# Optimization experiments

Hardware: AMD Instinct MI355X
Metric: run time of the kernel (lower is better)

## Reference

```python
import jax, jax.numpy as jnp
import numpy as np

N = 100000      # nodes_num
E = 1600000     # edges (avg degree 16)
D_IN = 256
D_OUT = 128
EPS = 1e-3      # keras BatchNormalization default epsilon
LEAKY = 0.2     # tf.nn.leaky_relu default alpha


def setup_inputs() -> dict:
    key = jax.random.key(0)
    ks = jax.random.split(key, 6)
    x = jax.random.normal(ks[0], (N, D_IN), jnp.float32)
    w = jax.random.normal(ks[1], (D_IN, D_OUT), jnp.float32) / np.float32(np.sqrt(D_IN))
    w1 = jax.random.normal(ks[2], (D_IN, D_IN), jnp.float32) / np.float32(np.sqrt(D_IN))
    w2 = jax.random.normal(ks[3], (D_IN, D_IN), jnp.float32) / np.float32(np.sqrt(D_IN))
    rows = jnp.sort(jax.random.randint(ks[4], (E,), 0, N, jnp.int32))
    cols = jax.random.randint(ks[5], (E,), 0, N, jnp.int32)
    edge_vals = jnp.ones((E,), jnp.float32)
    return {"x": x, "w": w, "w1": w1, "w2": w2,
            "edge_vals": edge_vals, "rows": rows, "cols": cols}


def reference(x, w, w1, w2, edge_vals, rows, cols):
    # Batch norm (training mode: per-feature stats over node axis, gamma=1, beta=0)
    mean = jnp.mean(x, axis=0)
    var = jnp.var(x, axis=0)
    xn = (x - mean) * jax.lax.rsqrt(var + EPS)          # [N, D_IN]

    mapped = xn @ w                                      # [N, D_OUT]
    s1 = jnp.tanh(jnp.sum((xn @ w1) * xn, axis=1))       # [N] row score
    s2 = jnp.tanh(jnp.sum((xn @ w2) * xn, axis=1))       # [N] col score

    # sparse add of adj*s1[row] and adj*s2[col], then leaky_relu on edge values
    ev = edge_vals * (s1[rows] + s2[cols])               # [E]
    ev = jnp.where(ev > 0, ev, LEAKY * ev)

    # tf.sparse.softmax: softmax over the nonzero entries of each row
    m = jax.ops.segment_max(ev, rows, num_segments=N)    # [N]
    m = jnp.where(jnp.isfinite(m), m, 0.0)               # empty rows -> 0
    ex = jnp.exp(ev - m[rows])
    denom = jax.ops.segment_sum(ex, rows, num_segments=N)
    alpha = ex / denom[rows]                             # [E] edge softmax

    # SpMM: out[i] = sum_{e: rows[e]==i} alpha[e] * mapped[cols[e]]
    out = jax.ops.segment_sum(alpha[:, None] * mapped[cols], rows, num_segments=N)
    return out  # activation is identity (activation=None)
```

## Files before the change

### kernel.cpp

```cpp
#include <hip/hip_runtime.h>

#define D_IN 256
#define D_OUT 128
#define EPS_BN 1e-3f
#define LEAKY 0.2f

typedef unsigned short u16;
typedef unsigned int u32;
typedef u16 u16x4 __attribute__((ext_vector_type(4)));
typedef u16 u16x8 __attribute__((ext_vector_type(8)));
typedef __bf16 bf16x8 __attribute__((ext_vector_type(8)));
typedef float f32x4 __attribute__((ext_vector_type(4)));

__device__ __forceinline__ float bf2f(u16 u) {
    u32 v = ((u32)u) << 16;
    return __uint_as_float(v);
}
__device__ __forceinline__ u16 f2bf(float f) {
    u32 u = __float_as_uint(f);
    u32 r = (u + 0x7FFFu + ((u >> 16) & 1u)) >> 16;
    return (u16)r;
}

__device__ __forceinline__ void bar_lgkm() {
    asm volatile("s_waitcnt lgkmcnt(0)" ::: "memory");
    __builtin_amdgcn_s_barrier();
    asm volatile("" ::: "memory");
}

__global__ void colstats_k(const float* __restrict__ x, int n,
                           float* __restrict__ sums, float* __restrict__ sqs) {
    int c = threadIdx.x;
    float s = 0.f, q = 0.f;
    for (int r = blockIdx.x; r < n; r += gridDim.x) {
        float v = x[(size_t)r * D_IN + c];
        s += v;
        q += v * v;
    }
    atomicAdd(&sums[c], s);
    atomicAdd(&sqs[c], q);
}

__global__ void finalize_k(const float* __restrict__ sums, const float* __restrict__ sqs,
                           int n, float* __restrict__ mean, float* __restrict__ inv) {
    int c = threadIdx.x;
    float m = sums[c] / (float)n;
    float v = sqs[c] / (float)n - m * m;
    mean[c] = m;
    inv[c] = rsqrtf(v + EPS_BN);
}

__global__ void prep_w_k(const float* __restrict__ w1, const float* __restrict__ w2,
                         const float* __restrict__ w, u16* __restrict__ Bth,
                         u16* __restrict__ Btl, u16* __restrict__ Wth,
                         u16* __restrict__ Wtl) {
    int idx = blockIdx.x * 256 + threadIdx.x;
    int k = idx & 255;
    int nn = idx >> 8;
    if (nn < 512) {
        float v = (nn < 256) ? w1[(size_t)k * 256 + nn]
                             : w2[(size_t)k * 256 + (nn - 256)];
        u16 h = f2bf(v);
        u16 l = f2bf(v - bf2f(h));
        Bth[(size_t)nn * 256 + k] = h;
        Btl[(size_t)nn * 256 + k] = l;
    } else {
        int nm = nn - 512;
        float v = w[(size_t)k * D_OUT + nm];
        u16 h = f2bf(v);
        u16 l = f2bf(v - bf2f(h));
        Wth[(size_t)nm * 256 + k] = h;
        Wtl[(size_t)nm * 256 + k] = l;
    }
}

__device__ __forceinline__ int kmap(int v, int g, int j) {
    return (v == 0) ? (8 * g + j) : (16 * (j >> 2) + 4 * g + (j & 3));
}

__global__ void probe_k(int* __restrict__ flagp) {
    __shared__ float Ar[16][32];
    __shared__ float Br[32][16];
    __shared__ float Dr[16][16];
    int l = threadIdx.x;
    for (int i = l; i < 512; i += 64) {
        int r = i >> 5, k = i & 31;
        Ar[r][k] = (float)(((r * 5 + k * 3) % 11) - 5);
    }
    for (int i = l; i < 512; i += 64) {
        int k = i >> 4, c = i & 15;
        Br[k][c] = (float)(((k * 3 + c * 7) % 13) - 6);
    }
    __syncthreads();
    for (int i = l; i < 256; i += 64) {
        int r = i >> 4, c = i & 15;
        float s = 0.f;
        for (int k = 0; k < 32; ++k) s += Ar[r][k] * Br[k][c];
        Dr[r][c] = s;
    }
    __syncthreads();
    int g = l >> 4, c15 = l & 15;
    int found = -1;
    for (int combo = 0; combo < 4; ++combo) {
        int va = combo >> 1, vb = combo & 1;
        u16x8 af, bfv;
#pragma unroll
        for (int j = 0; j < 8; ++j) {
            af[j] = f2bf(Ar[c15][kmap(va, g, j)]);
            bfv[j] = f2bf(Br[kmap(vb, g, j)][c15]);
        }
        f32x4 d = {0.f, 0.f, 0.f, 0.f};
        d = __builtin_amdgcn_mfma_f32_16x16x32_bf16(
            __builtin_bit_cast(bf16x8, af), __builtin_bit_cast(bf16x8, bfv), d,
            0, 0, 0);
        bool ok = true;
#pragma unroll
        for (int r = 0; r < 4; ++r) ok = ok && (d[r] == Dr[g * 4 + r][c15]);
        if (found < 0 && __all(ok)) found = combo;
    }
    if (l == 0) flagp[0] = (found < 0) ? 0 : found;
}

template <int NT>
__device__ __forceinline__ void stage_A(const float* __restrict__ x,
                                        const float* __restrict__ mean,
                                        const float* __restrict__ inv, int m0,
                                        int n, u16* Ah, u16* Al) {
    const int tid = threadIdx.x;
#pragma unroll
    for (int i = 0; i < 4096 / NT; ++i) {
        int chunk = tid + i * NT;
        int r = chunk >> 6;
        int c4 = (chunk & 63) << 2;
        int gr = m0 + r;
        bool ok = gr < n;
        float4 v = make_float4(0.f, 0.f, 0.f, 0.f);
        if (ok) v = *(const float4*)(x + (size_t)gr * D_IN + c4);
        float4 mn = *(const float4*)(mean + c4);
        float4 iv = *(const float4*)(inv + c4);
        float a0 = ok ? (v.x - mn.x) * iv.x : 0.f;
        float a1 = ok ? (v.y - mn.y) * iv.y : 0.f;
        float a2 = ok ? (v.z - mn.z) * iv.z : 0.f;
        float a3 = ok ? (v.w - mn.w) * iv.w : 0.f;
        u16 h0 = f2bf(a0), h1 = f2bf(a1), h2 = f2bf(a2), h3 = f2bf(a3);
        u16 l0 = f2bf(a0 - bf2f(h0)), l1 = f2bf(a1 - bf2f(h1));
        u16 l2 = f2bf(a2 - bf2f(h2)), l3 = f2bf(a3 - bf2f(h3));
        int off = (r << 9) + (((c4 << 1) ^ ((r & 7) << 4)));
        u16x4 hv = {h0, h1, h2, h3};
        u16x4 lv = {l0, l1, l2, l3};
        *(u16x4*)((char*)Ah + off) = hv;
        *(u16x4*)((char*)Al + off) = lv;
    }
}

template <int V>
__device__ __forceinline__ bf16x8 ld_frag(const u16* plane, int rowByteBase,
                                          int swz, int kbyte, int g) {
    const char* p = (const char*)plane + rowByteBase;
    if constexpr (V == 0) {
        u16x8 v = *(const u16x8*)(p + ((kbyte + (g << 4)) ^ swz));
        return __builtin_bit_cast(bf16x8, v);
    } else {
        u16x4 a = *(const u16x4*)(p + ((kbyte + (g << 3)) ^ swz));
        u16x4 b = *(const u16x4*)(p + ((kbyte + 32 + (g << 3)) ^ swz));
        u16x8 v;
        v[0] = a[0]; v[1] = a[1]; v[2] = a[2]; v[3] = a[3];
        v[4] = b[0]; v[5] = b[1]; v[6] = b[2]; v[7] = b[3];
        return __builtin_bit_cast(bf16x8, v);
    }
}

__device__ __forceinline__ void ldb2(const u16* __restrict__ Gh,
                                     const u16* __restrict__ Gl, int n0, int k0,
                                     int tid, u16x8 (&hv)[2], u16x8 (&lv)[2]) {
#pragma unroll
    for (int i = 0; i < 2; ++i) {
        int chunk = tid + (i << 8);
        int nl = chunk >> 2;
        int k8 = (chunk & 3) << 3;
        size_t goff = (size_t)(n0 + nl) * 256 + k0 + k8;
        hv[i] = *(const u16x8*)(Gh + goff);
        lv[i] = *(const u16x8*)(Gl + goff);
    }
}
__device__ __forceinline__ void stb2(u16* Bh, u16* Bl, int tid,
                                     const u16x8 (&hv)[2], const u16x8 (&lv)[2]) {
#pragma unroll
    for (int i = 0; i < 2; ++i) {
        int chunk = tid + (i << 8);
        int nl = chunk >> 2;
        int kb = (chunk & 3) << 4;
        int off = (nl << 6) + (kb ^ (((nl >> 1) & 3) << 4));
        *(u16x8*)((char*)Bh + off) = hv[i];
        *(u16x8*)((char*)Bl + off) = lv[i];
    }
}
template <int V>
__device__ __forceinline__ bf16x8 ld_bfrag(const u16* Bp, int nl, int g) {
    const char* p = (const char*)Bp + (nl << 6);
    int swz = ((nl >> 1) & 3) << 4;
    if constexpr (V == 0) {
        u16x8 v = *(const u16x8*)(p + ((g << 4) ^ swz));
        return __builtin_bit_cast(bf16x8, v);
    } else {
        u16x4 a = *(const u16x4*)(p + ((g << 3) ^ swz));
        u16x4 b = *(const u16x4*)(p + ((32 + (g << 3)) ^ swz));
        u16x8 v;
        v[0] = a[0]; v[1] = a[1]; v[2] = a[2]; v[3] = a[3];
        v[4] = b[0]; v[5] = b[1]; v[6] = b[2]; v[7] = b[3];
        return __builtin_bit_cast(bf16x8, v);
    }
}

template <int VA, int VB>
__device__ __forceinline__ void comp32(const u16* Ah, const u16* Al,
                                       const u16* Bh, const u16* Bl, int kbA,
                                       int wm, int wj, int c15, int g,
                                       f32x4 (&acc)[2][4]) {
    bf16x8 ah[2], alf[2];
#pragma unroll
    for (int mf = 0; mf < 2; ++mf) {
        int row = wm * 32 + mf * 16 + c15;
        int swz = (row & 7) << 4;
        ah[mf] = ld_frag<VA>(Ah, row << 9, swz, kbA, g);
        alf[mf] = ld_frag<VA>(Al, row << 9, swz, kbA, g);
    }
    bf16x8 bh[4], bl[4];
#pragma unroll
    for (int nf = 0; nf < 4; ++nf) {
        int nl = wj * 64 + nf * 16 + c15;
        bh[nf] = ld_bfrag<VB>(Bh, nl, g);
        bl[nf] = ld_bfrag<VB>(Bl, nl, g);
    }
#pragma unroll
    for (int mf = 0; mf < 2; ++mf)
#pragma unroll
        for (int nf = 0; nf < 4; ++nf) {
            acc[mf][nf] = __builtin_amdgcn_mfma_f32_16x16x32_bf16(
                ah[mf], bh[nf], acc[mf][nf], 0, 0, 0);
            acc[mf][nf] = __builtin_amdgcn_mfma_f32_16x16x32_bf16(
                ah[mf], bl[nf], acc[mf][nf], 0, 0, 0);
            acc[mf][nf] = __builtin_amdgcn_mfma_f32_16x16x32_bf16(
                alf[mf], bh[nf], acc[mf][nf], 0, 0, 0);
        }
}

__device__ __forceinline__ void nxt_src2(int u, int totSub,
                                         const u16* __restrict__ Bth,
                                         const u16* __restrict__ Btl,
                                         const u16* __restrict__ Wth,
                                         const u16* __restrict__ Wtl,
                                         const u16*& Gh, const u16*& Gl,
                                         int& n0, int& k0) {
    if (u >= totSub) u = totSub - 1;
    if (u < 32) {
        Gh = Bth; Gl = Btl;
        n0 = (u >> 3) << 7;
        k0 = (u & 7) << 5;
    } else {
        Gh = Wth; Gl = Wtl;
        n0 = 0;
        k0 = (u & 7) << 5;
    }
}

template <int VA, int VB>
__device__ __forceinline__ void quadmap_body(
    const float* __restrict__ x, const u16* __restrict__ Bth,
    const u16* __restrict__ Btl, const u16* __restrict__ Wth,
    const u16* __restrict__ Wtl, const float* __restrict__ mean,
    const float* __restrict__ inv, float* __restrict__ s1,
    float* __restrict__ s2, u16* __restrict__ mapped, int n, int mapCT,
    u16* Ah, u16* Al, u16* Bh, u16* Bl) {
    const int tid = threadIdx.x;
    const int lane = tid & 63, wave = tid >> 6;
    const int g = lane >> 4, c15 = lane & 15;
    const int wm = wave >> 1, wj = wave & 1;
    const int m0 = blockIdx.x * 64;

    stage_A<256>(x, mean, inv, m0, n, Ah, Al);
    __syncthreads();

    const int totSub = 32 + ((mapCT == 128) ? 8 : 0);
    u16x8 rh[2], rl[2];
    {
        const u16 *Gh, *Gl; int n0, k0;
        nxt_src2(0, totSub, Bth, Btl, Wth, Wtl, Gh, Gl, n0, k0);
        ldb2(Gh, Gl, n0, k0, tid, rh, rl);
    }

    float sp[2][4] = {{0.f, 0.f, 0.f, 0.f}, {0.f, 0.f, 0.f, 0.f}};
    float* red = (float*)Bh;

    for (int p = 0; p < 4; ++p) {
        f32x4 acc[2][4];
#pragma unroll
        for (int mf = 0; mf < 2; ++mf)
#pragma unroll
            for (int nf = 0; nf < 4; ++nf) acc[mf][nf] = (f32x4){0.f, 0.f, 0.f, 0.f};

#pragma unroll
        for (int u8 = 0; u8 < 8; ++u8) {
            bar_lgkm();
            stb2(Bh, Bl, tid, rh, rl);
            const u16 *Gh, *Gl; int n0, k0;
            nxt_src2(p * 8 + u8 + 1, totSub, Bth, Btl, Wth, Wtl, Gh, Gl, n0, k0);
            ldb2(Gh, Gl, n0, k0, tid, rh, rl);
            bar_lgkm();
            comp32<VA, VB>(Ah, Al, Bh, Bl, u8 * 64, wm, wj, c15, g, acc);
        }

        {
            int jtg = p * 2 + wj;
            int fcol0 = (jtg & 3) << 6;
#pragma unroll
            for (int nf = 0; nf < 4; ++nf) {
                int col = fcol0 + nf * 16 + c15;
                float mn = mean[col], ivv = inv[col];
#pragma unroll
                for (int mf = 0; mf < 2; ++mf) {
#pragma unroll
                    for (int r = 0; r < 4; ++r) {
                        int grow = m0 + wm * 32 + mf * 16 + g * 4 + r;
                        float xv = 0.f;
                        if (grow < n) xv = (x[(size_t)grow * D_IN + col] - mn) * ivv;
                        sp[mf][r] = fmaf(acc[mf][nf][r], xv, sp[mf][r]);
                    }
                }
            }
        }
        if (p & 1) {
            float part[2][4];
#pragma unroll
            for (int mf = 0; mf < 2; ++mf)
#pragma unroll
                for (int r = 0; r < 4; ++r) {
                    float v = sp[mf][r];
                    v += __shfl_xor(v, 1);
                    v += __shfl_xor(v, 2);
                    v += __shfl_xor(v, 4);
                    v += __shfl_xor(v, 8);
                    part[mf][r] = v;
                    sp[mf][r] = 0.f;
                }
            bar_lgkm();
            if (c15 == 0) {
#pragma unroll
                for (int mf = 0; mf < 2; ++mf)
#pragma unroll
                    for (int r = 0; r < 4; ++r) {
                        int sidx = (((((wm << 2) | g) << 1) | mf) << 3) | (r << 1) | wj;
                        red[sidx] = part[mf][r];
                    }
            }
            bar_lgkm();
            if (wj == 0 && c15 == 0) {
                float* dst = (p < 2) ? s1 : s2;
#pragma unroll
                for (int mf = 0; mf < 2; ++mf)
#pragma unroll
                    for (int r = 0; r < 4; ++r) {
                        int sidx = (((((wm << 2) | g) << 1) | mf) << 3) | (r << 1);
                        float tot = red[sidx] + red[sidx | 1];
                        int grow = m0 + wm * 32 + mf * 16 + g * 4 + r;
                        if (grow < n) dst[grow] = tanhf(tot);
                    }
            }
        }
    }

    if (mapCT == 128) {
        f32x4 acc[2][4];
#pragma unroll
        for (int mf = 0; mf < 2; ++mf)
#pragma unroll
            for (int nf = 0; nf < 4; ++nf) acc[mf][nf] = (f32x4){0.f, 0.f, 0.f, 0.f};

#pragma unroll
        for (int u8 = 0; u8 < 8; ++u8) {
            bar_lgkm();
            stb2(Bh, Bl, tid, rh, rl);
            const u16 *Gh, *Gl; int n0, k0;
            nxt_src2(32 + u8 + 1, totSub, Bth, Btl, Wth, Wtl, Gh, Gl, n0, k0);
            ldb2(Gh, Gl, n0, k0, tid, rh, rl);
            bar_lgkm();
            comp32<VA, VB>(Ah, Al, Bh, Bl, u8 * 64, wm, wj, c15, g, acc);
        }
#pragma unroll
        for (int mf = 0; mf < 2; ++mf)
#pragma unroll
            for (int nf = 0; nf < 4; ++nf) {
                int si = wj * 64 + nf * 16 + c15;
#pragma unroll
                for (int r = 0; r < 4; ++r) {
                    int grow = m0 + wm * 32 + mf * 16 + g * 4 + r;
                    if (grow < n)
                        mapped[(size_t)grow * 128 + si] = f2bf(acc[mf][nf][r]);
                }
            }
    }
}

__global__ __launch_bounds__(256) void quadmap_mfma_k(
    const float* __restrict__ x, const u16* __restrict__ Bth,
    const u16* __restrict__ Btl, const u16* __restrict__ Wth,
    const u16* __restrict__ Wtl, const float* __restrict__ mean,
    const float* __restrict__ inv, float* __restrict__ s1,
    float* __restrict__ s2, u16* __restrict__ mapped,
    const int* __restrict__ flagp, int n, int mapCT) {
    __shared__ u16 Ah[64 * 256];
    __shared__ u16 Al[64 * 256];
    __shared__ u16 Bh[128 * 32];
    __shared__ u16 Bl[128 * 32];
    int v = flagp[0];
    if (v == 1)
        quadmap_body<0, 1>(x, Bth, Btl, Wth, Wtl, mean, inv, s1, s2, mapped, n, mapCT, Ah, Al, Bh, Bl);
    else if (v == 2)
        quadmap_body<1, 0>(x, Bth, Btl, Wth, Wtl, mean, inv, s1, s2, mapped, n, mapCT, Ah, Al, Bh, Bl);
    else if (v == 3)
        quadmap_body<1, 1>(x, Bth, Btl, Wth, Wtl, mean, inv, s1, s2, mapped, n, mapCT, Ah, Al, Bh, Bl);
    else
        quadmap_body<0, 0>(x, Bth, Btl, Wth, Wtl, mean, inv, s1, s2, mapped, n, mapCT, Ah, Al, Bh, Bl);
}

__device__ __forceinline__ void ldb_regs(const u16* __restrict__ Gh,
                                         const u16* __restrict__ Gl, int n0,
                                         int k0, int tid, u16x8 (&hv)[2],
                                         u16x8 (&lv)[2]) {
#pragma unroll
    for (int i = 0; i < 2; ++i) {
        int chunk = tid + (i << 8);
        int nl = chunk >> 3;
        int k8 = (chunk & 7) << 3;
        size_t goff = (size_t)(n0 + nl) * 256 + k0 + k8;
        hv[i] = *(const u16x8*)(Gh + goff);
        lv[i] = *(const u16x8*)(Gl + goff);
    }
}
__device__ __forceinline__ void stb_lds(u16* Bh, u16* Bl, int tid,
                                        const u16x8 (&hv)[2],
                                        const u16x8 (&lv)[2]) {
#pragma unroll
    for (int i = 0; i < 2; ++i) {
        int chunk = tid + (i << 8);
        int nl = chunk >> 3;
        int k8 = (chunk & 7) << 3;
        int off = (nl << 7) + (((k8 << 1) ^ ((nl & 7) << 4)));
        *(u16x8*)((char*)Bh + off) = hv[i];
        *(u16x8*)((char*)Bl + off) = lv[i];
    }
}
template <int VA, int VB>
__device__ __forceinline__ void comp_kt(const u16* Ah, const u16* Al,
                                        const u16* Bh, const u16* Bl, int kt,
                                        int wm, int wn, int c15, int g,
                                        f32x4 (&acc)[2][2]) {
#pragma unroll
    for (int kk = 0; kk < 2; ++kk) {
        int kbA = kt * 128 + kk * 64;
        int kbB = kk * 64;
        bf16x8 ah[2], alf[2], bhf[2], blf[2];
#pragma unroll
        for (int mf = 0; mf < 2; ++mf) {
            int row = wm * 32 + mf * 16 + c15;
            int swz = (row & 7) << 4;
            ah[mf] = ld_frag<VA>(Ah, row << 9, swz, kbA, g);
            alf[mf] = ld_frag<VA>(Al, row << 9, swz, kbA, g);
        }
#pragma unroll
        for (int nf = 0; nf < 2; ++nf) {
            int nl = wn * 32 + nf * 16 + c15;
            int swz = (nl & 7) << 4;
            bhf[nf] = ld_frag<VB>(Bh, nl << 7, swz, kbB, g);
            blf[nf] = ld_frag<VB>(Bl, nl << 7, swz, kbB, g);
        }
#pragma unroll
        for (int mf = 0; mf < 2; ++mf)
#pragma unroll
            for (int nf = 0; nf < 2; ++nf) {
                acc[mf][nf] = __builtin_amdgcn_mfma_f32_16x16x32_bf16(
                    ah[mf], bhf[nf], acc[mf][nf], 0, 0, 0);
                acc[mf][nf] = __builtin_amdgcn_mfma_f32_16x16x32_bf16(
                    ah[mf], blf[nf], acc[mf][nf], 0, 0, 0);
                acc[mf][nf] = __builtin_amdgcn_mfma_f32_16x16x32_bf16(
                    alf[mf], bhf[nf], acc[mf][nf], 0, 0, 0);
            }
    }
}

template <int VA, int VB>
__device__ __forceinline__ void map_body(
    const float* __restrict__ x, const u16* __restrict__ Wth,
    const u16* __restrict__ Wtl, const float* __restrict__ mean,
    const float* __restrict__ inv, u16* __restrict__ mapped, int n, int c0,
    int CT, u16* Ah, u16* Al, u16* Bh, u16* Bl) {
    const int tid = threadIdx.x;
    const int lane = tid & 63, wave = tid >> 6;
    const int g = lane >> 4, c15 = lane & 15;
    const int wm = wave >> 1, wn = wave & 1;
    const int m0 = blockIdx.x * 64;

    stage_A<256>(x, mean, inv, m0, n, Ah, Al);
    __syncthreads();

    u16x8 rbh[2], rbl[2];
    ldb_regs(Wth, Wtl, c0, 0, tid, rbh, rbl);

    const int tiles = CT >> 6;
    for (int t = 0; t < tiles; ++t) {
        f32x4 acc[2][2];
#pragma unroll
        for (int mf = 0; mf < 2; ++mf)
#pragma unroll
            for (int nf = 0; nf < 2; ++nf) acc[mf][nf] = (f32x4){0.f, 0.f, 0.f, 0.f};

        for (int kt = 0; kt < 4; ++kt) {
            bar_lgkm();
            stb_lds(Bh, Bl, tid, rbh, rbl);
            int nn0 = (kt < 3) ? c0 + t * 64
                               : c0 + ((t + 1 < tiles) ? (t + 1) * 64 : t * 64);
            int nk0 = (kt < 3) ? (kt + 1) * 64 : 0;
            ldb_regs(Wth, Wtl, nn0, nk0, tid, rbh, rbl);
            bar_lgkm();
            comp_kt<VA, VB>(Ah, Al, Bh, Bl, kt, wm, wn, c15, g, acc);
        }
#pragma unroll
        for (int mf = 0; mf < 2; ++mf)
#pragma unroll
            for (int nf = 0; nf < 2; ++nf) {
                int si = t * 64 + wn * 32 + nf * 16 + c15;
#pragma unroll
                for (int r = 0; r < 4; ++r) {
                    int grow = m0 + wm * 32 + mf * 16 + g * 4 + r;
                    if (grow < n) mapped[(size_t)grow * CT + si] = f2bf(acc[mf][nf][r]);
                }
            }
    }
}

__global__ __launch_bounds__(256) void map_mfma_k(
    const float* __restrict__ x, const u16* __restrict__ Wth,
    const u16* __restrict__ Wtl, const float* __restrict__ mean,
    const float* __restrict__ inv, u16* __restrict__ mapped, int n, int c0,
    int CT, const int* __restrict__ flagp) {
    __shared__ u16 Ah[64 * 256];
    __shared__ u16 Al[64 * 256];
    __shared__ u16 Bh[64 * 64];
    __shared__ u16 Bl[64 * 64];
    int v = flagp[0];
    if (v == 1) map_body<0, 1>(x, Wth, Wtl, mean, inv, mapped, n, c0, CT, Ah, Al, Bh, Bl);
    else if (v == 2) map_body<1, 0>(x, Wth, Wtl, mean, inv, mapped, n, c0, CT, Ah, Al, Bh, Bl);
    else if (v == 3) map_body<1, 1>(x, Wth, Wtl, mean, inv, mapped, n, c0, CT, Ah, Al, Bh, Bl);
    else map_body<0, 0>(x, Wth, Wtl, mean, inv, mapped, n, c0, CT, Ah, Al, Bh, Bl);
}

template <typename OT>
__global__ __launch_bounds__(256) void gemm_map_k(const float* __restrict__ x,
                                                  const float* __restrict__ w,
                                                  const float* __restrict__ mean,
                                                  const float* __restrict__ inv,
                                                  OT* __restrict__ outp, int n,
                                                  int c0, int CT) {
    __shared__ float As[64][68];
    __shared__ float Bs[64][68];
    const int tid = threadIdx.x;
    const int tx = tid & 15, ty = tid >> 4;
    const int m0 = blockIdx.x * 64;
    const int tiles = (CT + 63) >> 6;

    for (int t = 0; t < tiles; ++t) {
        const int jt = c0 + (t << 6);
        float acc[4][4];
#pragma unroll
        for (int a = 0; a < 4; ++a)
#pragma unroll
            for (int b = 0; b < 4; ++b) acc[a][b] = 0.f;

        for (int kt = 0; kt < D_IN; kt += 64) {
#pragma unroll
            for (int i = 0; i < 4; ++i) {
                int f4 = tid + 256 * i;
                int r = f4 >> 4;
                int c4 = (f4 & 15) << 2;
                float4 o;
                int gr = m0 + r;
                if (gr < n) {
                    float4 v = *(const float4*)(x + (size_t)gr * D_IN + kt + c4);
                    float4 mn = *(const float4*)(mean + kt + c4);
                    float4 iv = *(const float4*)(inv + kt + c4);
                    o.x = (v.x - mn.x) * iv.x;
                    o.y = (v.y - mn.y) * iv.y;
                    o.z = (v.z - mn.z) * iv.z;
                    o.w = (v.w - mn.w) * iv.w;
                } else {
                    o = make_float4(0.f, 0.f, 0.f, 0.f);
                }
                *(float4*)&As[r][c4] = o;
            }
#pragma unroll
            for (int i = 0; i < 4; ++i) {
                int f4 = tid + 256 * i;
                int r = f4 >> 4;
                int c4 = (f4 & 15) << 2;
                int jc = jt + c4;
                float4 bv = (jc < D_OUT)
                                ? *(const float4*)(w + (size_t)(kt + r) * D_OUT + jc)
                                : make_float4(0.f, 0.f, 0.f, 0.f);
                *(float4*)&Bs[r][c4] = bv;
            }
            __syncthreads();
#pragma unroll 8
            for (int k = 0; k < 64; ++k) {
                float4 bv = *(const float4*)&Bs[k][tx << 2];
                float a0 = As[(ty << 2) + 0][k];
                float a1 = As[(ty << 2) + 1][k];
                float a2 = As[(ty << 2) + 2][k];
                float a3 = As[(ty << 2) + 3][k];
                acc[0][0] = fmaf(a0, bv.x, acc[0][0]);
                acc[0][1] = fmaf(a0, bv.y, acc[0][1]);
                acc[0][2] = fmaf(a0, bv.z, acc[0][2]);
                acc[0][3] = fmaf(a0, bv.w, acc[0][3]);
                acc[1][0] = fmaf(a1, bv.x, acc[1][0]);
                acc[1][1] = fmaf(a1, bv.y, acc[1][1]);
                acc[1][2] = fmaf(a1, bv.z, acc[1][2]);
                acc[1][3] = fmaf(a1, bv.w, acc[1][3]);
                acc[2][0] = fmaf(a2, bv.x, acc[2][0]);
                acc[2][1] = fmaf(a2, bv.y, acc[2][1]);
                acc[2][2] = fmaf(a2, bv.z, acc[2][2]);
                acc[2][3] = fmaf(a2, bv.w, acc[2][3]);
                acc[3][0] = fmaf(a3, bv.x, acc[3][0]);
                acc[3][1] = fmaf(a3, bv.y, acc[3][1]);
                acc[3][2] = fmaf(a3, bv.z, acc[3][2]);
                acc[3][3] = fmaf(a3, bv.w, acc[3][3]);
            }
            __syncthreads();
        }
        int si = (jt - c0) + (tx << 2);
        if (si < CT) {
#pragma unroll
            for (int a = 0; a < 4; ++a) {
                int gm = m0 + (ty << 2) + a;
                if (gm < n) {
                    ushort4 pk;
                    pk.x = f2bf(acc[a][0]);
                    pk.y = f2bf(acc[a][1]);
                    pk.z = f2bf(acc[a][2]);
                    pk.w = f2bf(acc[a][3]);
                    *(ushort4*)((u16*)outp + (size_t)gm * CT + si) = pk;
                }
            }
        }
    }
}

__global__ void build_rowptr_k(const int* __restrict__ rows, int E, int n,
                               int* __restrict__ rp) {
    int e = blockIdx.x * blockDim.x + threadIdx.x;
    if (e >= E) return;
    int r = rows[e];
    int prev = (e == 0) ? -1 : rows[e - 1];
    for (int q = prev + 1; q <= r; ++q) rp[q] = e;
    if (e == E - 1) {
        for (int q = r + 1; q <= n; ++q) rp[q] = E;
    }
}

template <bool WRITE_ALPHA>
__global__ __launch_bounds__(256) void row_softmax_k(
    const int* __restrict__ row_ptr, const int* __restrict__ cols,
    const float* __restrict__ ev, const float* __restrict__ s1,
    const float* __restrict__ s2, float* __restrict__ rmax,
    float* __restrict__ rsm, float* __restrict__ alpha, int n) {
    int wave = threadIdx.x >> 6;
    int lane = threadIdx.x & 63;
    int row = blockIdx.x * 4 + wave;
    if (row >= n) return;
    int e0 = row_ptr[row], e1 = row_ptr[row + 1];
    if (e0 >= e1) {
        if (lane == 0) {
            rmax[row] = 0.f;
            rsm[row] = 0.f;
        }
        return;
    }
    float s1r = s1[row];
    float mx = -1e30f;
    for (int e = e0 + lane; e < e1; e += 64) {
        float v = ev[e] * (s1r + s2[cols[e]]);
        v = v > 0.f ? v : LEAKY * v;
        mx = fmaxf(mx, v);
    }
#pragma unroll
    for (int off = 32; off; off >>= 1) mx = fmaxf(mx, __shfl_xor(mx, off));
    float sm = 0.f;
    for (int e = e0 + lane; e < e1; e += 64) {
        float v = ev[e] * (s1r + s2[cols[e]]);
        v = v > 0.f ? v : LEAKY * v;
        sm += __expf(v - mx);
    }
#pragma unroll
    for (int off = 32; off; off >>= 1) sm += __shfl_xor(sm, off);
    float rsm_v = 1.f / sm;
    if (lane == 0) {
        rmax[row] = mx;
        rsm[row] = rsm_v;
    }
    if constexpr (WRITE_ALPHA) {
        for (int e = e0 + lane; e < e1; e += 64) {
            float v = ev[e] * (s1r + s2[cols[e]]);
            v = v > 0.f ? v : LEAKY * v;
            alpha[e] = __expf(v - mx) * rsm_v;
        }
    }
}

template <bool HAS_ALPHA>
__global__ __launch_bounds__(256) void attn_gather2_k(
    const int* __restrict__ row_ptr, const int* __restrict__ cols,
    const float* __restrict__ alpha, const float* __restrict__ ev,
    const float* __restrict__ s1, const float* __restrict__ s2,
    const float* __restrict__ rmax, const float* __restrict__ rsm,
    const u16* __restrict__ mapped, float* __restrict__ outp, int n, int c0,
    int CT) {
    const int wave = threadIdx.x >> 6;
    const int lane = threadIdx.x & 63;
    const int row = blockIdx.x * 4 + wave;
    if (row >= n) return;
    const int e0 = row_ptr[row], e1 = row_ptr[row + 1];
    float* orow = outp + (size_t)row * D_OUT + c0;
    const int nu = CT >> 1;
    const bool act = lane < nu;
    if (e0 >= e1) {
        if (act) *(float2*)(orow + (lane << 1)) = make_float2(0.f, 0.f);
        return;
    }
    float s1r = 0.f, mxv = 0.f, rsv = 0.f;
    if constexpr (!HAS_ALPHA) {
        s1r = s1[row];
        mxv = rmax[row];
        rsv = rsm[row];
    }
    const u32* map32 = (const u32*)mapped;
    float ox = 0.f, oy = 0.f;
    int e = e0;
    while (e < e1) {
        int cnt = min(e1 - e, 64);
        int ce = 0;
        float ae = 0.f;
        if (lane < cnt) {
            int ee = e + lane;
            ce = cols[ee];
            if constexpr (HAS_ALPHA) {
                ae = alpha[ee];
            } else {
                float v = ev[ee] * (s1r + s2[ce]);
                v = v > 0.f ? v : LEAKY * v;
                ae = __expf(v - mxv) * rsv;
            }
        }
        for (int j0 = 0; j0 < cnt; j0 += 8) {
            int cv[8];
            float av[8];
            u32 mv[8];
#pragma unroll
            for (int j = 0; j < 8; ++j) {
                cv[j] = __shfl(ce, j0 + j);
                av[j] = __shfl(ae, j0 + j);
            }
#pragma unroll
            for (int j = 0; j < 8; ++j)
                mv[j] = act ? map32[(size_t)cv[j] * nu + lane] : 0u;
#pragma unroll
            for (int j = 0; j < 8; ++j) {
                ox = fmaf(av[j], bf2f((u16)(mv[j] & 0xffffu)), ox);
                oy = fmaf(av[j], bf2f((u16)(mv[j] >> 16)), oy);
            }
        }
        e += cnt;
    }
    if (act) *(float2*)(orow + (lane << 1)) = make_float2(ox, oy);
}

extern "C" void kernel_launch(void* const* d_in, const int* in_sizes, int n_in,
                              void* d_out, int out_size, void* d_ws, size_t ws_size,
                              hipStream_t stream) {
    const float* x  = (const float*)d_in[0];
    const float* w  = (const float*)d_in[1];
    const float* w1 = (const float*)d_in[2];
    const float* w2 = (const float*)d_in[3];
    const float* ev = (const float*)d_in[4];
    const int* rows = (const int*)d_in[5];
    const int* cols = (const int*)d_in[6];
    float* out = (float*)d_out;

    const int N = in_sizes[0] / D_IN;
    const int E = in_sizes[4];

    char* base = (char*)d_ws;
    size_t off = 0;
    auto alloc = [&](size_t bytes) -> char* {
        off = (off + 255) & ~(size_t)255;
        char* p = base + off;
        off += bytes;
        return p;
    };
    float* sums  = (float*)alloc(256 * 4);
    float* sqs   = (float*)alloc(256 * 4);
    float* mean  = (float*)alloc(256 * 4);
    float* inv   = (float*)alloc(256 * 4);
    float* s1    = (float*)alloc((size_t)N * 4);
    float* s2    = (float*)alloc((size_t)N * 4);
    float* rmax  = (float*)alloc((size_t)N * 4);
    float* rsm   = (float*)alloc((size_t)N * 4);
    int* row_ptr = (int*)alloc((size_t)(N + 1) * 4);
    int* flag    = (int*)alloc(256);
    u16* Bth = (u16*)alloc((size_t)512 * 256 * 2);
    u16* Btl = (u16*)alloc((size_t)512 * 256 * 2);
    u16* Wth = (u16*)alloc((size_t)128 * 256 * 2);
    u16* Wtl = (u16*)alloc((size_t)128 * 256 * 2);
    size_t head0 = off;

    size_t alpha_bytes = (size_t)E * 4;
    auto fits_alpha = [&](size_t mapped_bytes) {
        size_t o = (head0 + 255) & ~(size_t)255;
        o += alpha_bytes;
        o = (o + 255) & ~(size_t)255;
        return o + mapped_bytes <= ws_size;
    };
    auto fits_noalpha = [&](size_t mapped_bytes) {
        size_t o = (head0 + 255) & ~(size_t)255;
        return o + mapped_bytes <= ws_size;
    };

    bool has_alpha;
    int CT;
    if (fits_alpha((size_t)N * 128 * 2)) {
        has_alpha = true; CT = 128;
    } else if (fits_alpha((size_t)N * 64 * 2)) {
        has_alpha = true; CT = 64;
    } else if (fits_noalpha((size_t)N * 32 * 2)) {
        has_alpha = false; CT = 32;
    } else if (fits_noalpha((size_t)N * 16 * 2)) {
        has_alpha = false; CT = 16;
    } else {
        has_alpha = false; CT = 8;
    }
    float* alpha = has_alpha ? (float*)alloc(alpha_bytes) : nullptr;
    u16* mapped = (u16*)alloc((size_t)N * CT * 2);

    hipMemsetAsync(sums, 0, 512 * sizeof(float), stream);
    colstats_k<<<512, 256, 0, stream>>>(x, N, sums, sqs);
    finalize_k<<<1, 256, 0, stream>>>(sums, sqs, N, mean, inv);
    prep_w_k<<<640, 256, 0, stream>>>(w1, w2, w, Bth, Btl, Wth, Wtl);
    probe_k<<<1, 64, 0, stream>>>(flag);

    int qb = (N + 63) / 64;
    int mapCT = (CT == 128) ? 128 : 0;
    quadmap_mfma_k<<<qb, 256, 0, stream>>>(x, Bth, Btl, Wth, Wtl, mean, inv, s1,
                                           s2, mapped, flag, N, mapCT);

    build_rowptr_k<<<(E + 255) / 256, 256, 0, stream>>>(rows, E, N, row_ptr);
    int ab = (N + 3) / 4;
    if (has_alpha) {
        row_softmax_k<true><<<ab, 256, 0, stream>>>(row_ptr, cols, ev, s1, s2,
                                                    rmax, rsm, alpha, N);
    } else {
        row_softmax_k<false><<<ab, 256, 0, stream>>>(row_ptr, cols, ev, s1, s2,
                                                     rmax, rsm, nullptr, N);
    }

    if (CT == 128) {
        attn_gather2_k<true><<<ab, 256, 0, stream>>>(
            row_ptr, cols, alpha, ev, s1, s2, rmax, rsm, mapped, out, N, 0, CT);
    } else if (CT == 64) {
        map_mfma_k<<<qb, 256, 0, stream>>>(x, Wth, Wtl, mean, inv, mapped, N, 0,
                                           64, flag);
        attn_gather2_k<true><<<ab, 256, 0, stream>>>(
            row_ptr, cols, alpha, ev, s1, s2, rmax, rsm, mapped, out, N, 0, 64);
        map_mfma_k<<<qb, 256, 0, stream>>>(x, Wth, Wtl, mean, inv, mapped, N, 64,
                                           64, flag);
        attn_gather2_k<true><<<ab, 256, 0, stream>>>(
            row_ptr, cols, alpha, ev, s1, s2, rmax, rsm, mapped, out, N, 64, 64);
    } else {
        for (int c0 = 0; c0 < D_OUT; c0 += CT) {
            gemm_map_k<u16><<<qb, 256, 0, stream>>>(x, w, mean, inv, mapped, N,
                                                    c0, CT);
            attn_gather2_k<false><<<ab, 256, 0, stream>>>(
                row_ptr, cols, nullptr, ev, s1, s2, rmax, rsm, mapped, out, N,
                c0, CT);
        }
    }
}
```

Baseline: 581.2 us.

## Switch split-bf16 GEMMs to fp16 with scaled low-part weights

Replaces the three-term bf16 hi/lo split product with fp16. A is now stored as a single fp16 plane, and the weights keep a hi part plus a low residual scaled by 2048, each accumulated separately and combined at the end. This cuts MFMA count from three to two per tile, removes the A low-plane LDS staging, and halves A shared memory, which may also raise occupancy. In exchange it relies on fp16 range and precision for the normalized activations, which is riskier if values overflow or lose accuracy.

```diff
diff --git a/kernel.cpp b/kernel.cpp
--- a/kernel.cpp
+++ b/kernel.cpp
@@ -9,7 +9,8 @@
 typedef unsigned int u32;
 typedef u16 u16x4 __attribute__((ext_vector_type(4)));
 typedef u16 u16x8 __attribute__((ext_vector_type(8)));
-typedef __bf16 bf16x8 __attribute__((ext_vector_type(8)));
+typedef _Float16 f16;
+typedef f16 f16x8 __attribute__((ext_vector_type(8)));
 typedef float f32x4 __attribute__((ext_vector_type(4)));
 
 __device__ __forceinline__ float bf2f(u16 u) {
@@ -20,6 +21,10 @@
     u32 u = __float_as_uint(f);
     u32 r = (u + 0x7FFFu + ((u >> 16) & 1u)) >> 16;
     return (u16)r;
+}
+__device__ __forceinline__ u16 f2h(float f) {
+    f16 h = (f16)f;
+    return __builtin_bit_cast(u16, h);
 }
 
 __device__ __forceinline__ void bar_lgkm() {
@@ -57,21 +62,23 @@
     int idx = blockIdx.x * 256 + threadIdx.x;
     int k = idx & 255;
     int nn = idx >> 8;
+    float v;
+    u16* dh;
+    u16* dl;
+    size_t o;
     if (nn < 512) {
-        float v = (nn < 256) ? w1[(size_t)k * 256 + nn]
-                             : w2[(size_t)k * 256 + (nn - 256)];
-        u16 h = f2bf(v);
-        u16 l = f2bf(v - bf2f(h));
-        Bth[(size_t)nn * 256 + k] = h;
-        Btl[(size_t)nn * 256 + k] = l;
+        v = (nn < 256) ? w1[(size_t)k * 256 + nn] : w2[(size_t)k * 256 + (nn - 256)];
+        dh = Bth; dl = Btl; o = (size_t)nn * 256 + k;
     } else {
         int nm = nn - 512;
-        float v = w[(size_t)k * D_OUT + nm];
-        u16 h = f2bf(v);
-        u16 l = f2bf(v - bf2f(h));
-        Wth[(size_t)nm * 256 + k] = h;
-        Wtl[(size_t)nm * 256 + k] = l;
-    }
+        v = w[(size_t)k * D_OUT + nm];
+        dh = Wth; dl = Wtl; o = (size_t)nm * 256 + k;
+    }
+    f16 h = (f16)v;
+    float hf = (float)h;
+    f16 l = (f16)((v - hf) * 2048.0f);
+    dh[o] = __builtin_bit_cast(u16, h);
+    dl[o] = __builtin_bit_cast(u16, l);
 }
 
 __device__ __forceinline__ int kmap(int v, int g, int j) {
@@ -103,16 +110,14 @@
     int found = -1;
     for (int combo = 0; combo < 4; ++combo) {
         int va = combo >> 1, vb = combo & 1;
-        u16x8 af, bfv;
+        f16x8 af, bfv;
 #pragma unroll
         for (int j = 0; j < 8; ++j) {
-            af[j] = f2bf(Ar[c15][kmap(va, g, j)]);
-            bfv[j] = f2bf(Br[kmap(vb, g, j)][c15]);
+            af[j] = (f16)Ar[c15][kmap(va, g, j)];
+            bfv[j] = (f16)Br[kmap(vb, g, j)][c15];
         }
         f32x4 d = {0.f, 0.f, 0.f, 0.f};
-        d = __builtin_amdgcn_mfma_f32_16x16x32_bf16(
-            __builtin_bit_cast(bf16x8, af), __builtin_bit_cast(bf16x8, bfv), d,
-            0, 0, 0);
+        d = __builtin_amdgcn_mfma_f32_16x16x32_f16(af, bfv, d, 0, 0, 0);
         bool ok = true;
 #pragma unroll
         for (int r = 0; r < 4; ++r) ok = ok && (d[r] == Dr[g * 4 + r][c15]);
@@ -125,7 +130,7 @@
 __device__ __forceinline__ void stage_A(const float* __restrict__ x,
                                         const float* __restrict__ mean,
                                         const float* __restrict__ inv, int m0,
-                                        int n, u16* Ah, u16* Al) {
+                                        int n, u16* Ah) {
     const int tid = threadIdx.x;
 #pragma unroll
     for (int i = 0; i < 4096 / NT; ++i) {
@@ -142,31 +147,26 @@
         float a1 = ok ? (v.y - mn.y) * iv.y : 0.f;
         float a2 = ok ? (v.z - mn.z) * iv.z : 0.f;
         float a3 = ok ? (v.w - mn.w) * iv.w : 0.f;
-        u16 h0 = f2bf(a0), h1 = f2bf(a1), h2 = f2bf(a2), h3 = f2bf(a3);
-        u16 l0 = f2bf(a0 - bf2f(h0)), l1 = f2bf(a1 - bf2f(h1));
-        u16 l2 = f2bf(a2 - bf2f(h2)), l3 = f2bf(a3 - bf2f(h3));
         int off = (r << 9) + (((c4 << 1) ^ ((r & 7) << 4)));
-        u16x4 hv = {h0, h1, h2, h3};
-        u16x4 lv = {l0, l1, l2, l3};
+        u16x4 hv = {f2h(a0), f2h(a1), f2h(a2), f2h(a3)};
         *(u16x4*)((char*)Ah + off) = hv;
-        *(u16x4*)((char*)Al + off) = lv;
     }
 }
 
 template <int V>
-__device__ __forceinline__ bf16x8 ld_frag(const u16* plane, int rowByteBase,
-                                          int swz, int kbyte, int g) {
+__device__ __forceinline__ f16x8 ld_frag(const u16* plane, int rowByteBase,
+                                         int swz, int kbyte, int g) {
     const char* p = (const char*)plane + rowByteBase;
     if constexpr (V == 0) {
         u16x8 v = *(const u16x8*)(p + ((kbyte + (g << 4)) ^ swz));
-        return __builtin_bit_cast(bf16x8, v);
+        return __builtin_bit_cast(f16x8, v);
     } else {
         u16x4 a = *(const u16x4*)(p + ((kbyte + (g << 3)) ^ swz));
         u16x4 b = *(const u16x4*)(p + ((kbyte + 32 + (g << 3)) ^ swz));
         u16x8 v;
         v[0] = a[0]; v[1] = a[1]; v[2] = a[2]; v[3] = a[3];
         v[4] = b[0]; v[5] = b[1]; v[6] = b[2]; v[7] = b[3];
-        return __builtin_bit_cast(bf16x8, v);
+        return __builtin_bit_cast(f16x8, v);
     }
 }
 
@@ -196,36 +196,35 @@
     }
 }
 template <int V>
-__device__ __forceinline__ bf16x8 ld_bfrag(const u16* Bp, int nl, int g) {
+__device__ __forceinline__ f16x8 ld_bfrag(const u16* Bp, int nl, int g) {
     const char* p = (const char*)Bp + (nl << 6);
     int swz = ((nl >> 1) & 3) << 4;
     if constexpr (V == 0) {
         u16x8 v = *(const u16x8*)(p + ((g << 4) ^ swz));
-        return __builtin_bit_cast(bf16x8, v);
+        return __builtin_bit_cast(f16x8, v);
     } else {
         u16x4 a = *(const u16x4*)(p + ((g << 3) ^ swz));
         u16x4 b = *(const u16x4*)(p + ((32 + (g << 3)) ^ swz));
         u16x8 v;
         v[0] = a[0]; v[1] = a[1]; v[2] = a[2]; v[3] = a[3];
         v[4] = b[0]; v[5] = b[1]; v[6] = b[2]; v[7] = b[3];
-        return __builtin_bit_cast(bf16x8, v);
+        return __builtin_bit_cast(f16x8, v);
     }
 }
 
 template <int VA, int VB>
-__device__ __forceinline__ void comp32(const u16* Ah, const u16* Al,
-                                       const u16* Bh, const u16* Bl, int kbA,
-                                       int wm, int wj, int c15, int g,
-                                       f32x4 (&acc)[2][4]) {
-    bf16x8 ah[2], alf[2];
+__device__ __forceinline__ void comp32(const u16* Ah, const u16* Bh,
+                                       const u16* Bl, int kbA, int wm, int wj,
+                                       int c15, int g, f32x4 (&accH)[2][4],
+                                       f32x4 (&accL)[2][4]) {
+    f16x8 ah[2];
 #pragma unroll
     for (int mf = 0; mf < 2; ++mf) {
         int row = wm * 32 + mf * 16 + c15;
         int swz = (row & 7) << 4;
         ah[mf] = ld_frag<VA>(Ah, row << 9, swz, kbA, g);
-        alf[mf] = ld_frag<VA>(Al, row << 9, swz, kbA, g);
-    }
-    bf16x8 bh[4], bl[4];
+    }
+    f16x8 bh[4], bl[4];
 #pragma unroll
     for (int nf = 0; nf < 4; ++nf) {
         int nl = wj * 64 + nf * 16 + c15;
@@ -236,12 +235,10 @@
     for (int mf = 0; mf < 2; ++mf)
 #pragma unroll
         for (int nf = 0; nf < 4; ++nf) {
-            acc[mf][nf] = __builtin_amdgcn_mfma_f32_16x16x32_bf16(
-                ah[mf], bh[nf], acc[mf][nf], 0, 0, 0);
-            acc[mf][nf] = __builtin_amdgcn_mfma_f32_16x16x32_bf16(
-                ah[mf], bl[nf], acc[mf][nf], 0, 0, 0);
-            acc[mf][nf] = __builtin_amdgcn_mfma_f32_16x16x32_bf16(
-                alf[mf], bh[nf], acc[mf][nf], 0, 0, 0);
+            accH[mf][nf] = __builtin_amdgcn_mfma_f32_16x16x32_f16(
+                ah[mf], bh[nf], accH[mf][nf], 0, 0, 0);
+            accL[mf][nf] = __builtin_amdgcn_mfma_f32_16x16x32_f16(
+                ah[mf], bl[nf], accL[mf][nf], 0, 0, 0);
         }
 }
 
@@ -271,14 +268,15 @@
     const u16* __restrict__ Wtl, const float* __restrict__ mean,
     const float* __restrict__ inv, float* __restrict__ s1,
     float* __restrict__ s2, u16* __restrict__ mapped, int n, int mapCT,
-    u16* Ah, u16* Al, u16* Bh, u16* Bl) {
+    u16* Ah, u16* Bh, u16* Bl) {
     const int tid = threadIdx.x;
     const int lane = tid & 63, wave = tid >> 6;
     const int g = lane >> 4, c15 = lane & 15;
     const int wm = wave >> 1, wj = wave & 1;
     const int m0 = blockIdx.x * 64;
-
-    stage_A<256>(x, mean, inv, m0, n, Ah, Al);
+    const float LS = 1.0f / 2048.0f;
+
+    stage_A<256>(x, mean, inv, m0, n, Ah);
     __syncthreads();
 
     const int totSub = 32 + ((mapCT == 128) ? 8 : 0);
@@ -293,11 +291,14 @@
     float* red = (float*)Bh;
 
     for (int p = 0; p < 4; ++p) {
-        f32x4 acc[2][4];
+        f32x4 accH[2][4], accL[2][4];
 #pragma unroll
         for (int mf = 0; mf < 2; ++mf)
 #pragma unroll
-            for (int nf = 0; nf < 4; ++nf) acc[mf][nf] = (f32x4){0.f, 0.f, 0.f, 0.f};
+            for (int nf = 0; nf < 4; ++nf) {
+                accH[mf][nf] = (f32x4){0.f, 0.f, 0.f, 0.f};
+                accL[mf][nf] = (f32x4){0.f, 0.f, 0.f, 0.f};
+            }
 
 #pragma unroll
         for (int u8 = 0; u8 < 8; ++u8) {
@@ -307,7 +308,7 @@
             nxt_src2(p * 8 + u8 + 1, totSub, Bth, Btl, Wth, Wtl, Gh, Gl, n0, k0);
             ldb2(Gh, Gl, n0, k0, tid, rh, rl);
             bar_lgkm();
-            comp32<VA, VB>(Ah, Al, Bh, Bl, u8 * 64, wm, wj, c15, g, acc);
+            comp32<VA, VB>(Ah, Bh, Bl, u8 * 64, wm, wj, c15, g, accH, accL);
         }
 
         {
@@ -324,7 +325,8 @@
                         int grow = m0 + wm * 32 + mf * 16 + g * 4 + r;
                         float xv = 0.f;
                         if (grow < n) xv = (x[(size_t)grow * D_IN + col] - mn) * ivv;
-                        sp[mf][r] = fmaf(acc[mf][nf][r], xv, sp[mf][r]);
+                        float y = fmaf(accL[mf][nf][r], LS, accH[mf][nf][r]);
+                        sp[mf][r] = fmaf(y, xv, sp[mf][r]);
                     }
                 }
             }
@@ -370,11 +372,14 @@
     }
 
     if (mapCT == 128) {
-        f32x4 acc[2][4];
+        f32x4 accH[2][4], accL[2][4];
 #pragma unroll
         for (int mf = 0; mf < 2; ++mf)
 #pragma unroll
-            for (int nf = 0; nf < 4; ++nf) acc[mf][nf] = (f32x4){0.f, 0.f, 0.f, 0.f};
+            for (int nf = 0; nf < 4; ++nf) {
+                accH[mf][nf] = (f32x4){0.f, 0.f, 0.f, 0.f};
+                accL[mf][nf] = (f32x4){0.f, 0.f, 0.f, 0.f};
+            }
 
 #pragma unroll
         for (int u8 = 0; u8 < 8; ++u8) {
@@ -384,7 +389,7 @@
             nxt_src2(32 + u8 + 1, totSub, Bth, Btl, Wth, Wtl, Gh, Gl, n0, k0);
             ldb2(Gh, Gl, n0, k0, tid, rh, rl);
             bar_lgkm();
-            comp32<VA, VB>(Ah, Al, Bh, Bl, u8 * 64, wm, wj, c15, g, acc);
+            comp32<VA, VB>(Ah, Bh, Bl, u8 * 64, wm, wj, c15, g, accH, accL);
         }
 #pragma unroll
         for (int mf = 0; mf < 2; ++mf)
@@ -394,8 +399,10 @@
 #pragma unroll
                 for (int r = 0; r < 4; ++r) {
                     int grow = m0 + wm * 32 + mf * 16 + g * 4 + r;
-                    if (grow < n)
-                        mapped[(size_t)grow * 128 + si] = f2bf(acc[mf][nf][r]);
+                    if (grow < n) {
+                        float y = fmaf(accL[mf][nf][r], LS, accH[mf][nf][r]);
+                        mapped[(size_t)grow * 128 + si] = f2bf(y);
+                    }
                 }
             }
     }
@@ -409,18 +416,17 @@
     float* __restrict__ s2, u16* __restrict__ mapped,
     const int* __restrict__ flagp, int n, int mapCT) {
     __shared__ u16 Ah[64 * 256];
-    __shared__ u16 Al[64 * 256];
     __shared__ u16 Bh[128 * 32];
     __shared__ u16 Bl[128 * 32];
     int v = flagp[0];
     if (v == 1)
-        quadmap_body<0, 1>(x, Bth, Btl, Wth, Wtl, mean, inv, s1, s2, mapped, n, mapCT, Ah, Al, Bh, Bl);
+        quadmap_body<0, 1>(x, Bth, Btl, Wth, Wtl, mean, inv, s1, s2, mapped, n, mapCT, Ah, Bh, Bl);
     else if (v == 2)
-        quadmap_body<1, 0>(x, Bth, Btl, Wth, Wtl, mean, inv, s1, s2, mapped, n, mapCT, Ah, Al, Bh, Bl);
+        quadmap_body<1, 0>(x, Bth, Btl, Wth, Wtl, mean, inv, s1, s2, mapped, n, mapCT, Ah, Bh, Bl);
     else if (v == 3)
-        quadmap_body<1, 1>(x, Bth, Btl, Wth, Wtl, mean, inv, s1, s2, mapped, n, mapCT, Ah, Al, Bh, Bl);
+        quadmap_body<1, 1>(x, Bth, Btl, Wth, Wtl, mean, inv, s1, s2, mapped, n, mapCT, Ah, Bh, Bl);
     else
-        quadmap_body<0, 0>(x, Bth, Btl, Wth, Wtl, mean, inv, s1, s2, mapped, n, mapCT, Ah, Al, Bh, Bl);
+        quadmap_body<0, 0>(x, Bth, Btl, Wth, Wtl, mean, inv, s1, s2, mapped, n, mapCT, Ah, Bh, Bl);
 }
 
 __device__ __forceinline__ void ldb_regs(const u16* __restrict__ Gh,
@@ -451,21 +457,20 @@
     }
 }
 template <int VA, int VB>
-__device__ __forceinline__ void comp_kt(const u16* Ah, const u16* Al,
-                                        const u16* Bh, const u16* Bl, int kt,
-                                        int wm, int wn, int c15, int g,
-                                        f32x4 (&acc)[2][2]) {
+__device__ __forceinline__ void comp_kt(const u16* Ah, const u16* Bh,
+                                        const u16* Bl, int kt, int wm, int wn,
+                                        int c15, int g, f32x4 (&accH)[2][2],
+                                        f32x4 (&accL)[2][2]) {
 #pragma unroll
     for (int kk = 0; kk < 2; ++kk) {
         int kbA = kt * 128 + kk * 64;
         int kbB = kk * 64;
-        bf16x8 ah[2], alf[2], bhf[2], blf[2];
+        f16x8 ah[2], bhf[2], blf[2];
 #pragma unroll
         for (int mf = 0; mf < 2; ++mf) {
             int row = wm * 32 + mf * 16 + c15;
             int swz = (row & 7) << 4;
             ah[mf] = ld_frag<VA>(Ah, row << 9, swz, kbA, g);
-            alf[mf] = ld_frag<VA>(Al, row << 9, swz, kbA, g);
         }
 #pragma unroll
         for (int nf = 0; nf < 2; ++nf) {
@@ -478,12 +483,10 @@
         for (int mf = 0; mf < 2; ++mf)
 #pragma unroll
             for (int nf = 0; nf < 2; ++nf) {
-                acc[mf][nf] = __builtin_amdgcn_mfma_f32_16x16x32_bf16(
-                    ah[mf], bhf[nf], acc[mf][nf], 0, 0, 0);
-                acc[mf][nf] = __builtin_amdgcn_mfma_f32_16x16x32_bf16(
-                    ah[mf], blf[nf], acc[mf][nf], 0, 0, 0);
-                acc[mf][nf] = __builtin_amdgcn_mfma_f32_16x16x32_bf16(
-                    alf[mf], bhf[nf], acc[mf][nf], 0, 0, 0);
+                accH[mf][nf] = __builtin_amdgcn_mfma_f32_16x16x32_f16(
+                    ah[mf], bhf[nf], accH[mf][nf], 0, 0, 0);
+                accL[mf][nf] = __builtin_amdgcn_mfma_f32_16x16x32_f16(
+                    ah[mf], blf[nf], accL[mf][nf], 0, 0, 0);
             }
     }
 }
@@ -493,14 +496,15 @@
     const float* __restrict__ x, const u16* __restrict__ Wth,
     const u16* __restrict__ Wtl, const float* __restrict__ mean,
     const float* __restrict__ inv, u16* __restrict__ mapped, int n, int c0,
-    int CT, u16* Ah, u16* Al, u16* Bh, u16* Bl) {
+    int CT, u16* Ah, u16* Bh, u16* Bl) {
     const int tid = threadIdx.x;
     const int lane = tid & 63, wave = tid >> 6;
     const int g = lane >> 4, c15 = lane & 15;
     const int wm = wave >> 1, wn = wave & 1;
     const int m0 = blockIdx.x * 64;
-
-    stage_A<256>(x, mean, inv, m0, n, Ah, Al);
+    const float LS = 1.0f / 2048.0f;
+
+    stage_A<256>(x, mean, inv, m0, n, Ah);
     __syncthreads();
 
     u16x8 rbh[2], rbl[2];
@@ -508,11 +512,14 @@
 
     const int tiles = CT >> 6;
     for (int t = 0; t < tiles; ++t) {
-        f32x4 acc[2][2];
+        f32x4 accH[2][2], accL[2][2];
 #pragma unroll
         for (int mf = 0; mf < 2; ++mf)
 #pragma unroll
-            for (int nf = 0; nf < 2; ++nf) acc[mf][nf] = (f32x4){0.f, 0.f, 0.f, 0.f};
+            for (int nf = 0; nf < 2; ++nf) {
+                accH[mf][nf] = (f32x4){0.f, 0.f, 0.f, 0.f};
+                accL[mf][nf] = (f32x4){0.f, 0.f, 0.f, 0.f};
+            }
 
         for (int kt = 0; kt < 4; ++kt) {
             bar_lgkm();
@@ -522,7 +529,7 @@
             int nk0 = (kt < 3) ? (kt + 1) * 64 : 0;
             ldb_regs(Wth, Wtl, nn0, nk0, tid, rbh, rbl);
             bar_lgkm();
-            comp_kt<VA, VB>(Ah, Al, Bh, Bl, kt, wm, wn, c15, g, acc);
+            comp_kt<VA, VB>(Ah, Bh, Bl, kt, wm, wn, c15, g, accH, accL);
         }
 #pragma unroll
         for (int mf = 0; mf < 2; ++mf)
@@ -532,7 +539,10 @@
 #pragma unroll
                 for (int r = 0; r < 4; ++r) {
                     int grow = m0 + wm * 32 + mf * 16 + g * 4 + r;
-                    if (grow < n) mapped[(size_t)grow * CT + si] = f2bf(acc[mf][nf][r]);
+                    if (grow < n) {
+                        float y = fmaf(accL[mf][nf][r], LS, accH[mf][nf][r]);
+                        mapped[(size_t)grow * CT + si] = f2bf(y);
+                    }
                 }
             }
     }
@@ -544,14 +554,13 @@
     const float* __restrict__ inv, u16* __restrict__ mapped, int n, int c0,
     int CT, const int* __restrict__ flagp) {
     __shared__ u16 Ah[64 * 256];
-    __shared__ u16 Al[64 * 256];
     __shared__ u16 Bh[64 * 64];
     __shared__ u16 Bl[64 * 64];
     int v = flagp[0];
-    if (v == 1) map_body<0, 1>(x, Wth, Wtl, mean, inv, mapped, n, c0, CT, Ah, Al, Bh, Bl);
-    else if (v == 2) map_body<1, 0>(x, Wth, Wtl, mean, inv, mapped, n, c0, CT, Ah, Al, Bh, Bl);
-    else if (v == 3) map_body<1, 1>(x, Wth, Wtl, mean, inv, mapped, n, c0, CT, Ah, Al, Bh, Bl);
-    else map_body<0, 0>(x, Wth, Wtl, mean, inv, mapped, n, c0, CT, Ah, Al, Bh, Bl);
+    if (v == 1) map_body<0, 1>(x, Wth, Wtl, mean, inv, mapped, n, c0, CT, Ah, Bh, Bl);
+    else if (v == 2) map_body<1, 0>(x, Wth, Wtl, mean, inv, mapped, n, c0, CT, Ah, Bh, Bl);
+    else if (v == 3) map_body<1, 1>(x, Wth, Wtl, mean, inv, mapped, n, c0, CT, Ah, Bh, Bl);
+    else map_body<0, 0>(x, Wth, Wtl, mean, inv, mapped, n, c0, CT, Ah, Bh, Bl);
 }
 
 template <typename OT>
```

After: 664.7 us. 1.14x slower.
